# Optimization experiments

Measured on AMD Instinct MI355X. Metric: run time of the kernel, lower is better.

## Reference

```python
import jax, jax.numpy as jnp
import numpy as np

N = 100000   # nodes
E = 1600000  # edges (avg degree 16)
DN = 16      # node_attr_dim
DE = 8       # edge_attr_dim
H = 32       # node_emb_dim
L = 7        # num_gnn_layers


def setup_inputs() -> dict:
    key = jax.random.key(0)
    ks = jax.random.split(key, 8)
    s = 0.05
    return {
        "x": jax.random.normal(ks[0], (N, DN), jnp.float32),
        "edge_attr": jax.random.normal(ks[1], (E, DE), jnp.float32),
        "edge_index": jax.random.randint(ks[2], (2, E), 0, N),
        # node_init_mlp: Linear(DN -> H)
        "W_node": jax.random.normal(ks[3], (DN, H), jnp.float32) * s,
        "b_node": jnp.zeros((H,), jnp.float32),
        # per-layer message_mlp: Linear(H+DE -> H)
        "Wm": jax.random.normal(ks[4], (L, H + DE, H), jnp.float32) * s,
        "bm": jnp.zeros((L, H), jnp.float32),
        # per-layer update_mlp: Linear(H -> H) followed by ReLU
        "Wu": jax.random.normal(ks[5], (L, H, H), jnp.float32) * s,
        "bu": jnp.zeros((L, H), jnp.float32),
        # post_mlp: Linear(H -> 1)
        "W_post": jax.random.normal(ks[6], (H, 1), jnp.float32) * s,
        "b_post": jnp.zeros((1,), jnp.float32),
    }


def reference(x, edge_attr, edge_index, W_node, b_node, Wm, bm, Wu, bu, W_post, b_post):
    src = edge_index[0]  # x_j (source)
    dst = edge_index[1]  # aggregation index (target, PyG source_to_target)

    h = x @ W_node + b_node  # node_init_mlp: [N, H]

    def layer(h, params):
        Wm_l, bm_l, Wu_l, bu_l = params
        # message: concat([x_j, edge_attr]) -> Linear (extended_message_in_flag=False)
        msg_in = jnp.concatenate([h[src], edge_attr], axis=-1)  # [E, H+DE]
        msg = msg_in @ Wm_l + bm_l                              # [E, H]
        # aggregate: scatter-max onto target nodes
        aggr = jax.ops.segment_max(msg, dst, num_segments=N)    # [N, H]
        aggr = jnp.where(jnp.isneginf(aggr), 0.0, aggr)         # empty segments -> 0
        # update: ReLU(Linear(aggr)) (update_with_target_flag=False)
        upd = jax.nn.relu(aggr @ Wu_l + bu_l)
        # inter-layer bypass (residual)
        return h + upd, None

    h, _ = jax.lax.scan(layer, h, (Wm, bm, Wu, bu))
    return h @ W_post + b_post  # post_mlp: [N, 1]
```

## Files before the change

### kernel.cpp

```cpp
#include <hip/hip_runtime.h>

#define NN 100000
#define NE 1600000
#define DN 16
#define DE 8
#define H  32
#define NL 7

#define SCAN_BT   1024
#define SCAN_NB   ((NN + SCAN_BT - 1) / SCAN_BT)
#define BSUM_T    128


__global__ __launch_bounds__(256) void zero_cnt_kernel(int* __restrict__ cnt) {
    int i = blockIdx.x * blockDim.x + threadIdx.x;
    if (i < NN) cnt[i] = 0;
}

__global__ __launch_bounds__(256) void hist_kernel(const int* __restrict__ dst,
                                                   int* __restrict__ cnt) {
    int e = blockIdx.x * blockDim.x + threadIdx.x;
    if (e < NE) atomicAdd(&cnt[dst[e]], 1);
}

__global__ __launch_bounds__(SCAN_BT) void scan_partial_kernel(
        const int* __restrict__ cnt, int* __restrict__ bsum) {
    __shared__ int red[SCAN_BT];
    int t = threadIdx.x;
    int i = blockIdx.x * SCAN_BT + t;
    red[t] = (i < NN) ? cnt[i] : 0;
    __syncthreads();
    for (int off = SCAN_BT / 2; off > 0; off >>= 1) {
        if (t < off) red[t] += red[t + off];
        __syncthreads();
    }
    if (t == 0) bsum[blockIdx.x] = red[0];
}

__global__ __launch_bounds__(BSUM_T) void scan_bsum_kernel(
        const int* __restrict__ bsum, int* __restrict__ boff,
        int* __restrict__ rowstart ) {
    __shared__ int part[BSUM_T];
    int t = threadIdx.x;
    int v = (t < SCAN_NB) ? bsum[t] : 0;
    part[t] = v;
    __syncthreads();
    for (int off = 1; off < BSUM_T; off <<= 1) {
        int add = (t >= off) ? part[t - off] : 0;
        __syncthreads();
        part[t] += add;
        __syncthreads();
    }
    if (t < SCAN_NB) boff[t] = part[t] - v;
    if (t == BSUM_T - 1) rowstart[NN] = part[t];
}

__global__ __launch_bounds__(SCAN_BT) void scan_final_kernel(
        const int* __restrict__ cnt, const int* __restrict__ boff,
        int* __restrict__ rowstart, int* __restrict__ cursor) {
    __shared__ int part[SCAN_BT];
    int t = threadIdx.x;
    int i = blockIdx.x * SCAN_BT + t;
    int v = (i < NN) ? cnt[i] : 0;
    part[t] = v;
    __syncthreads();
    for (int off = 1; off < SCAN_BT; off <<= 1) {
        int add = (t >= off) ? part[t - off] : 0;
        __syncthreads();
        part[t] += add;
        __syncthreads();
    }
    if (i < NN) {
        int r = boff[blockIdx.x] + part[t] - v;
        rowstart[i] = r;
        cursor[i]   = r;
    }
}

template<int PERM>
__global__ __launch_bounds__(256) void scatter_kernel(
        const int* __restrict__ src, const int* __restrict__ dst,
        const float* __restrict__ ea,
        int* __restrict__ cursor,
        int* __restrict__ es, float* __restrict__ eas, int* __restrict__ eperm) {
    int e = blockIdx.x * blockDim.x + threadIdx.x;
    if (e >= NE) return;
    int pos = atomicAdd(&cursor[dst[e]], 1);
    es[pos] = src[e];
    if (PERM) {
        const float4* s4 = (const float4*)(ea + (long)e * DE);
        float4 a = s4[0], b = s4[1];
        float4* d4 = (float4*)(eas + (long)pos * DE);
        d4[0] = a; d4[1] = b;
    } else {
        eperm[pos] = e;
    }
}

__global__ __launch_bounds__(256) void init_kernel(
        const float* __restrict__ x,
        const float* __restrict__ W_node, const float* __restrict__ b_node,
        const float* __restrict__ Wm0, const float* __restrict__ bm0,
        float* __restrict__ h, float* __restrict__ hm)
{
    int n = blockIdx.x * blockDim.x + threadIdx.x;
    if (n >= NN) return;

    float xin[DN];
    #pragma unroll
    for (int k = 0; k < DN/4; ++k) {
        float4 v = ((const float4*)(x + (long)n*DN))[k];
        xin[4*k+0]=v.x; xin[4*k+1]=v.y; xin[4*k+2]=v.z; xin[4*k+3]=v.w;
    }
    float hv[H];
    #pragma unroll
    for (int j = 0; j < H; ++j) hv[j] = b_node[j];
    #pragma unroll
    for (int k = 0; k < DN; ++k)
        #pragma unroll
        for (int j = 0; j < H; ++j)
            hv[j] = fmaf(xin[k], W_node[k*H+j], hv[j]);

    #pragma unroll
    for (int j = 0; j < H/4; ++j)
        ((float4*)(h + (long)n*H))[j] = make_float4(hv[4*j],hv[4*j+1],hv[4*j+2],hv[4*j+3]);

    float hmv[H];
    #pragma unroll
    for (int j = 0; j < H; ++j) hmv[j] = bm0[j];
    #pragma unroll
    for (int k = 0; k < H; ++k)
        #pragma unroll
        for (int j = 0; j < H; ++j)
            hmv[j] = fmaf(hv[k], Wm0[k*H+j], hmv[j]);

    #pragma unroll
    for (int j = 0; j < H/4; ++j)
        ((float4*)(hm + (long)n*H))[j] = make_float4(hmv[4*j],hmv[4*j+1],hmv[4*j+2],hmv[4*j+3]);
}

template<int PERM>
__global__ __launch_bounds__(256) void aggr_kernel(
        const int* __restrict__ rowstart, const int* __restrict__ es,
        const float* __restrict__ eas,
        const float* __restrict__ ea,
        const int* __restrict__ eperm,
        const float* __restrict__ Wm_bot,
        const float* __restrict__ hm,
        float* __restrict__ aggr)
{
    int tid  = blockIdx.x * blockDim.x + threadIdx.x;
    int node = tid >> 4;
    int sub  = tid & 15;
    if (node >= NN) return;

    float w0[DE], w1[DE];
    #pragma unroll
    for (int k = 0; k < DE; ++k) {
        w0[k] = Wm_bot[k*H + sub*2 + 0];
        w1[k] = Wm_bot[k*H + sub*2 + 1];
    }

    float acc0 = -__builtin_inff(), acc1 = -__builtin_inff();

    int lo = rowstart[node], hi = rowstart[node+1];
    int i = lo;
    for (; i + 1 < hi; i += 2) {
        int s0 = es[i], s1 = es[i+1];
        const float4* p0;
        const float4* p1;
        if (PERM) {
            p0 = (const float4*)(eas + (long)i * DE);
            p1 = (const float4*)(eas + (long)(i+1) * DE);
        } else {
            p0 = (const float4*)(ea + (long)eperm[i] * DE);
            p1 = (const float4*)(ea + (long)eperm[i+1] * DE);
        }
        float2 hv0 = *(const float2*)(hm + (long)s0*H + sub*2);
        float2 hv1 = *(const float2*)(hm + (long)s1*H + sub*2);
        float4 a0 = p0[0], b0 = p0[1];
        float4 a1 = p1[0], b1 = p1[1];
        float m00 = hv0.x, m01 = hv0.y;
        float m10 = hv1.x, m11 = hv1.y;
        m00 = fmaf(a0.x, w0[0], m00);  m01 = fmaf(a0.x, w1[0], m01);
        m10 = fmaf(a1.x, w0[0], m10);  m11 = fmaf(a1.x, w1[0], m11);
        m00 = fmaf(a0.y, w0[1], m00);  m01 = fmaf(a0.y, w1[1], m01);
        m10 = fmaf(a1.y, w0[1], m10);  m11 = fmaf(a1.y, w1[1], m11);
        m00 = fmaf(a0.z, w0[2], m00);  m01 = fmaf(a0.z, w1[2], m01);
        m10 = fmaf(a1.z, w0[2], m10);  m11 = fmaf(a1.z, w1[2], m11);
        m00 = fmaf(a0.w, w0[3], m00);  m01 = fmaf(a0.w, w1[3], m01);
        m10 = fmaf(a1.w, w0[3], m10);  m11 = fmaf(a1.w, w1[3], m11);
        m00 = fmaf(b0.x, w0[4], m00);  m01 = fmaf(b0.x, w1[4], m01);
        m10 = fmaf(b1.x, w0[4], m10);  m11 = fmaf(b1.x, w1[4], m11);
        m00 = fmaf(b0.y, w0[5], m00);  m01 = fmaf(b0.y, w1[5], m01);
        m10 = fmaf(b1.y, w0[5], m10);  m11 = fmaf(b1.y, w1[5], m11);
        m00 = fmaf(b0.z, w0[6], m00);  m01 = fmaf(b0.z, w1[6], m01);
        m10 = fmaf(b1.z, w0[6], m10);  m11 = fmaf(b1.z, w1[6], m11);
        m00 = fmaf(b0.w, w0[7], m00);  m01 = fmaf(b0.w, w1[7], m01);
        m10 = fmaf(b1.w, w0[7], m10);  m11 = fmaf(b1.w, w1[7], m11);
        acc0 = fmaxf(acc0, fmaxf(m00, m10));
        acc1 = fmaxf(acc1, fmaxf(m01, m11));
    }
    if (i < hi) {
        int s0 = es[i];
        const float4* p0 = PERM ? (const float4*)(eas + (long)i * DE)
                                : (const float4*)(ea + (long)eperm[i] * DE);
        float2 hv0 = *(const float2*)(hm + (long)s0*H + sub*2);
        float4 a0 = p0[0], b0 = p0[1];
        float m00 = hv0.x, m01 = hv0.y;
        m00 = fmaf(a0.x, w0[0], m00);  m01 = fmaf(a0.x, w1[0], m01);
        m00 = fmaf(a0.y, w0[1], m00);  m01 = fmaf(a0.y, w1[1], m01);
        m00 = fmaf(a0.z, w0[2], m00);  m01 = fmaf(a0.z, w1[2], m01);
        m00 = fmaf(a0.w, w0[3], m00);  m01 = fmaf(a0.w, w1[3], m01);
        m00 = fmaf(b0.x, w0[4], m00);  m01 = fmaf(b0.x, w1[4], m01);
        m00 = fmaf(b0.y, w0[5], m00);  m01 = fmaf(b0.y, w1[5], m01);
        m00 = fmaf(b0.z, w0[6], m00);  m01 = fmaf(b0.z, w1[6], m01);
        m00 = fmaf(b0.w, w0[7], m00);  m01 = fmaf(b0.w, w1[7], m01);
        acc0 = fmaxf(acc0, m00);
        acc1 = fmaxf(acc1, m01);
    }
    if (lo == hi) { acc0 = 0.f; acc1 = 0.f; }
    *(float2*)(aggr + (long)node*H + sub*2) = make_float2(acc0, acc1);
}

__global__ __launch_bounds__(256) void update_kernel(
        const float* __restrict__ Wu, const float* __restrict__ bu,
        const float* __restrict__ Wm_next, const float* __restrict__ bm_next,
        const float* __restrict__ W_post, const float* __restrict__ b_post,
        float* __restrict__ h, float* __restrict__ hm,
        const float* __restrict__ aggr, float* __restrict__ out, int last)
{
    int n = blockIdx.x * blockDim.x + threadIdx.x;
    if (n >= NN) return;

    float av[H];
    #pragma unroll
    for (int j = 0; j < H/4; ++j) {
        float4 v = ((const float4*)(aggr + (long)n*H))[j];
        av[4*j+0]=v.x; av[4*j+1]=v.y; av[4*j+2]=v.z; av[4*j+3]=v.w;
    }

    float uv[H];
    #pragma unroll
    for (int j = 0; j < H; ++j) uv[j] = bu[j];
    #pragma unroll
    for (int k = 0; k < H; ++k)
        #pragma unroll
        for (int j = 0; j < H; ++j)
            uv[j] = fmaf(av[k], Wu[k*H+j], uv[j]);

    float hv[H];
    #pragma unroll
    for (int j = 0; j < H/4; ++j) {
        float4 v = ((const float4*)(h + (long)n*H))[j];
        hv[4*j+0]=v.x; hv[4*j+1]=v.y; hv[4*j+2]=v.z; hv[4*j+3]=v.w;
    }
    #pragma unroll
    for (int j = 0; j < H; ++j) hv[j] += fmaxf(uv[j], 0.f);

    #pragma unroll
    for (int j = 0; j < H/4; ++j)
        ((float4*)(h + (long)n*H))[j] = make_float4(hv[4*j],hv[4*j+1],hv[4*j+2],hv[4*j+3]);

    if (!last) {
        float hmv[H];
        #pragma unroll
        for (int j = 0; j < H; ++j) hmv[j] = bm_next[j];
        #pragma unroll
        for (int k = 0; k < H; ++k)
            #pragma unroll
            for (int j = 0; j < H; ++j)
                hmv[j] = fmaf(hv[k], Wm_next[k*H+j], hmv[j]);
        #pragma unroll
        for (int j = 0; j < H/4; ++j)
            ((float4*)(hm + (long)n*H))[j] = make_float4(hmv[4*j],hmv[4*j+1],hmv[4*j+2],hmv[4*j+3]);
    } else {
        float acc = b_post[0];
        #pragma unroll
        for (int k = 0; k < H; ++k) acc = fmaf(hv[k], W_post[k], acc);
        out[n] = acc;
    }
}

extern "C" void kernel_launch(void* const* d_in, const int* in_sizes, int n_in,
                              void* d_out, int out_size, void* d_ws, size_t ws_size,
                              hipStream_t stream)
{
    const float* x         = (const float*)d_in[0];
    const float* edge_attr = (const float*)d_in[1];
    const int*   edge_index= (const int*)  d_in[2];
    const float* W_node    = (const float*)d_in[3];
    const float* b_node    = (const float*)d_in[4];
    const float* Wm        = (const float*)d_in[5];
    const float* bm        = (const float*)d_in[6];
    const float* Wu        = (const float*)d_in[7];
    const float* bu        = (const float*)d_in[8];
    const float* W_post    = (const float*)d_in[9];
    const float* b_post    = (const float*)d_in[10];
    float* out = (float*)d_out;

    const int* src = edge_index;
    const int* dst = edge_index + NE;

    char* ws = (char*)d_ws;
    size_t off = 0;
    float* h        = (float*)(ws + off); off += (size_t)NN*H*4;
    float* hm       = (float*)(ws + off); off += (size_t)NN*H*4;
    float* aggr     = (float*)(ws + off); off += (size_t)NN*H*4;
    int*   cnt      = (int*)  (ws + off); off += (size_t)NN*4;
    int*   rowstart = (int*)  (ws + off); off += (size_t)(NN+16)*4;
    int*   cursor   = (int*)  (ws + off); off += (size_t)NN*4;
    int*   bsum     = (int*)  (ws + off); off += (size_t)256*4;
    int*   boff     = (int*)  (ws + off); off += (size_t)256*4;
    int*   es       = (int*)  (ws + off); off += (size_t)NE*4;
    size_t base = off;
    const int use_perm = (ws_size >= base + (size_t)NE*DE*4);
    float* eas   = (float*)(ws + base);
    int*   eperm = (int*)  (ws + base);

    const int nodeBlocks  = (NN + 255) / 256;
    const int edgeBlocks  = (NE + 255) / 256;
    const int aggrBlocks  = (NN*16 + 255) / 256;

    zero_cnt_kernel<<<nodeBlocks, 256, 0, stream>>>(cnt);
    hist_kernel<<<edgeBlocks, 256, 0, stream>>>(dst, cnt);
    scan_partial_kernel<<<SCAN_NB, SCAN_BT, 0, stream>>>(cnt, bsum);
    scan_bsum_kernel<<<1, BSUM_T, 0, stream>>>(bsum, boff, rowstart);
    scan_final_kernel<<<SCAN_NB, SCAN_BT, 0, stream>>>(cnt, boff, rowstart, cursor);
    if (use_perm)
        scatter_kernel<1><<<edgeBlocks, 256, 0, stream>>>(src, dst, edge_attr, cursor, es, eas, eperm);
    else
        scatter_kernel<0><<<edgeBlocks, 256, 0, stream>>>(src, dst, edge_attr, cursor, es, eas, eperm);

    init_kernel<<<nodeBlocks, 256, 0, stream>>>(x, W_node, b_node, Wm, bm, h, hm);

    for (int l = 0; l < NL; ++l) {
        const float* Wm_l   = Wm + (size_t)l*(H+DE)*H;
        const float* Wm_bot = Wm_l + (size_t)H*H;
        const float* Wu_l   = Wu + (size_t)l*H*H;
        const float* bu_l   = bu + (size_t)l*H;
        int last = (l == NL-1);
        const float* Wm_next = last ? nullptr : Wm + (size_t)(l+1)*(H+DE)*H;
        const float* bm_next = last ? nullptr : bm + (size_t)(l+1)*H;

        if (use_perm)
            aggr_kernel<1><<<aggrBlocks, 256, 0, stream>>>(rowstart, es, eas, edge_attr, eperm,
                                                           Wm_bot, hm, aggr);
        else
            aggr_kernel<0><<<aggrBlocks, 256, 0, stream>>>(rowstart, es, eas, edge_attr, eperm,
                                                           Wm_bot, hm, aggr);
        update_kernel<<<nodeBlocks, 256, 0, stream>>>(Wu_l, bu_l, Wm_next, bm_next,
                                                      W_post, b_post, h, hm, aggr, out, last);
    }
}
```

Before: 946.6 us.

## Fuse aggregation with update via subgroup shuffles; split scatter into index scatter and gather

Merges the per-layer aggregation and update kernels into one kernel. Each 16-lane group computes the node's Wu and next-layer Wm matmuls using __shfl broadcasts, which removes the aggr buffer round trip and one launch per layer. hm is double-buffered so the fused kernel can write the next layer's hm while other nodes still read the current one. When the workspace is large enough, the edge scatter is split into an atomic index-only scatter followed by a coalesced gather of src and edge_attr. This adds one extra edge pass and a permutation buffer.

```diff
diff --git a/kernel.cpp b/kernel.cpp
--- a/kernel.cpp
+++ b/kernel.cpp
@@ -77,24 +77,42 @@
     }
 }
 
-template<int PERM>
-__global__ __launch_bounds__(256) void scatter_kernel(
+__global__ __launch_bounds__(256) void scatter_idx_kernel(
+        const int* __restrict__ dst, int* __restrict__ cursor,
+        int* __restrict__ eperm) {
+    int e = blockIdx.x * blockDim.x + threadIdx.x;
+    if (e >= NE) return;
+    int pos = atomicAdd(&cursor[dst[e]], 1);
+    eperm[pos] = e;
+}
+
+__global__ __launch_bounds__(256) void gather_kernel(
+        const int* __restrict__ eperm, const int* __restrict__ src,
+        const float* __restrict__ ea,
+        int* __restrict__ es, float* __restrict__ eas) {
+    int i = blockIdx.x * blockDim.x + threadIdx.x;
+    if (i >= NE) return;
+    int e = eperm[i];
+    es[i] = src[e];
+    const float4* s4 = (const float4*)(ea + (long)e * DE);
+    float4 a = s4[0], b = s4[1];
+    float4* d4 = (float4*)(eas + (long)i * DE);
+    d4[0] = a; d4[1] = b;
+}
+
+__global__ __launch_bounds__(256) void scatter_combined_kernel(
         const int* __restrict__ src, const int* __restrict__ dst,
         const float* __restrict__ ea,
         int* __restrict__ cursor,
-        int* __restrict__ es, float* __restrict__ eas, int* __restrict__ eperm) {
+        int* __restrict__ es, float* __restrict__ eas) {
     int e = blockIdx.x * blockDim.x + threadIdx.x;
     if (e >= NE) return;
     int pos = atomicAdd(&cursor[dst[e]], 1);
     es[pos] = src[e];
-    if (PERM) {
-        const float4* s4 = (const float4*)(ea + (long)e * DE);
-        float4 a = s4[0], b = s4[1];
-        float4* d4 = (float4*)(eas + (long)pos * DE);
-        d4[0] = a; d4[1] = b;
-    } else {
-        eperm[pos] = e;
-    }
+    const float4* s4 = (const float4*)(ea + (long)e * DE);
+    float4 a = s4[0], b = s4[1];
+    float4* d4 = (float4*)(eas + (long)pos * DE);
+    d4[0] = a; d4[1] = b;
 }
 
 __global__ __launch_bounds__(256) void init_kernel(
@@ -139,15 +157,19 @@
         ((float4*)(hm + (long)n*H))[j] = make_float4(hmv[4*j],hmv[4*j+1],hmv[4*j+2],hmv[4*j+3]);
 }
 
-template<int PERM>
-__global__ __launch_bounds__(256) void aggr_kernel(
+template<int PERM, int LAST>
+__global__ __launch_bounds__(256) void aggr_update_kernel(
         const int* __restrict__ rowstart, const int* __restrict__ es,
         const float* __restrict__ eas,
         const float* __restrict__ ea,
         const int* __restrict__ eperm,
         const float* __restrict__ Wm_bot,
-        const float* __restrict__ hm,
-        float* __restrict__ aggr)
+        const float* __restrict__ hm_in,
+        const float* __restrict__ Wu, const float* __restrict__ bu,
+        const float* __restrict__ Wm_next, const float* __restrict__ bm_next,
+        const float* __restrict__ W_post, const float* __restrict__ b_post,
+        float* __restrict__ h, float* __restrict__ hm_out,
+        float* __restrict__ out)
 {
     int tid  = blockIdx.x * blockDim.x + threadIdx.x;
     int node = tid >> 4;
@@ -176,8 +198,8 @@
             p0 = (const float4*)(ea + (long)eperm[i] * DE);
             p1 = (const float4*)(ea + (long)eperm[i+1] * DE);
         }
-        float2 hv0 = *(const float2*)(hm + (long)s0*H + sub*2);
-        float2 hv1 = *(const float2*)(hm + (long)s1*H + sub*2);
+        float2 hv0 = *(const float2*)(hm_in + (long)s0*H + sub*2);
+        float2 hv1 = *(const float2*)(hm_in + (long)s1*H + sub*2);
         float4 a0 = p0[0], b0 = p0[1];
         float4 a1 = p1[0], b1 = p1[1];
         float m00 = hv0.x, m01 = hv0.y;
@@ -205,7 +227,7 @@
         int s0 = es[i];
         const float4* p0 = PERM ? (const float4*)(eas + (long)i * DE)
                                 : (const float4*)(ea + (long)eperm[i] * DE);
-        float2 hv0 = *(const float2*)(hm + (long)s0*H + sub*2);
+        float2 hv0 = *(const float2*)(hm_in + (long)s0*H + sub*2);
         float4 a0 = p0[0], b0 = p0[1];
         float m00 = hv0.x, m01 = hv0.y;
         m00 = fmaf(a0.x, w0[0], m00);  m01 = fmaf(a0.x, w1[0], m01);
@@ -220,65 +242,39 @@
         acc1 = fmaxf(acc1, m01);
     }
     if (lo == hi) { acc0 = 0.f; acc1 = 0.f; }
-    *(float2*)(aggr + (long)node*H + sub*2) = make_float2(acc0, acc1);
-}
-
-__global__ __launch_bounds__(256) void update_kernel(
-        const float* __restrict__ Wu, const float* __restrict__ bu,
-        const float* __restrict__ Wm_next, const float* __restrict__ bm_next,
-        const float* __restrict__ W_post, const float* __restrict__ b_post,
-        float* __restrict__ h, float* __restrict__ hm,
-        const float* __restrict__ aggr, float* __restrict__ out, int last)
-{
-    int n = blockIdx.x * blockDim.x + threadIdx.x;
-    if (n >= NN) return;
-
-    float av[H];
-    #pragma unroll
-    for (int j = 0; j < H/4; ++j) {
-        float4 v = ((const float4*)(aggr + (long)n*H))[j];
-        av[4*j+0]=v.x; av[4*j+1]=v.y; av[4*j+2]=v.z; av[4*j+3]=v.w;
-    }
-
-    float uv[H];
-    #pragma unroll
-    for (int j = 0; j < H; ++j) uv[j] = bu[j];
-    #pragma unroll
-    for (int k = 0; k < H; ++k)
+
+    float uv0 = bu[2*sub+0], uv1 = bu[2*sub+1];
+    #pragma unroll
+    for (int k = 0; k < 16; ++k) {
+        float a0 = __shfl(acc0, k, 16);
+        float a1 = __shfl(acc1, k, 16);
+        float2 wA = *(const float2*)(Wu + (2*k+0)*H + 2*sub);
+        float2 wB = *(const float2*)(Wu + (2*k+1)*H + 2*sub);
+        uv0 = fmaf(a0, wA.x, uv0); uv1 = fmaf(a0, wA.y, uv1);
+        uv0 = fmaf(a1, wB.x, uv0); uv1 = fmaf(a1, wB.y, uv1);
+    }
+    float2 hrow = *(const float2*)(h + (long)node*H + 2*sub);
+    float hv0 = hrow.x + fmaxf(uv0, 0.f);
+    float hv1 = hrow.y + fmaxf(uv1, 0.f);
+    *(float2*)(h + (long)node*H + 2*sub) = make_float2(hv0, hv1);
+
+    if (!LAST) {
+        float m0 = bm_next[2*sub+0], m1 = bm_next[2*sub+1];
         #pragma unroll
-        for (int j = 0; j < H; ++j)
-            uv[j] = fmaf(av[k], Wu[k*H+j], uv[j]);
-
-    float hv[H];
-    #pragma unroll
-    for (int j = 0; j < H/4; ++j) {
-        float4 v = ((const float4*)(h + (long)n*H))[j];
-        hv[4*j+0]=v.x; hv[4*j+1]=v.y; hv[4*j+2]=v.z; hv[4*j+3]=v.w;
-    }
-    #pragma unroll
-    for (int j = 0; j < H; ++j) hv[j] += fmaxf(uv[j], 0.f);
-
-    #pragma unroll
-    for (int j = 0; j < H/4; ++j)
-        ((float4*)(h + (long)n*H))[j] = make_float4(hv[4*j],hv[4*j+1],hv[4*j+2],hv[4*j+3]);
-
-    if (!last) {
-        float hmv[H];
+        for (int k = 0; k < 16; ++k) {
+            float a0 = __shfl(hv0, k, 16);
+            float a1 = __shfl(hv1, k, 16);
+            float2 wA = *(const float2*)(Wm_next + (2*k+0)*H + 2*sub);
+            float2 wB = *(const float2*)(Wm_next + (2*k+1)*H + 2*sub);
+            m0 = fmaf(a0, wA.x, m0); m1 = fmaf(a0, wA.y, m1);
+            m0 = fmaf(a1, wB.x, m0); m1 = fmaf(a1, wB.y, m1);
+        }
+        *(float2*)(hm_out + (long)node*H + 2*sub) = make_float2(m0, m1);
+    } else {
+        float p = hv0 * W_post[2*sub+0] + hv1 * W_post[2*sub+1];
         #pragma unroll
-        for (int j = 0; j < H; ++j) hmv[j] = bm_next[j];
-        #pragma unroll
-        for (int k = 0; k < H; ++k)
-            #pragma unroll
-            for (int j = 0; j < H; ++j)
-                hmv[j] = fmaf(hv[k], Wm_next[k*H+j], hmv[j]);
-        #pragma unroll
-        for (int j = 0; j < H/4; ++j)
-            ((float4*)(hm + (long)n*H))[j] = make_float4(hmv[4*j],hmv[4*j+1],hmv[4*j+2],hmv[4*j+3]);
-    } else {
-        float acc = b_post[0];
-        #pragma unroll
-        for (int k = 0; k < H; ++k) acc = fmaf(hv[k], W_post[k], acc);
-        out[n] = acc;
+        for (int o = 8; o >= 1; o >>= 1) p += __shfl_xor(p, o, 16);
+        if (sub == 0) out[node] = p + b_post[0];
     }
 }
 
@@ -305,8 +301,8 @@
     char* ws = (char*)d_ws;
     size_t off = 0;
     float* h        = (float*)(ws + off); off += (size_t)NN*H*4;
-    float* hm       = (float*)(ws + off); off += (size_t)NN*H*4;
-    float* aggr     = (float*)(ws + off); off += (size_t)NN*H*4;
+    float* hm0      = (float*)(ws + off); off += (size_t)NN*H*4;
+    float* hm1      = (float*)(ws + off); off += (size_t)NN*H*4;
     int*   cnt      = (int*)  (ws + off); off += (size_t)NN*4;
     int*   rowstart = (int*)  (ws + off); off += (size_t)(NN+16)*4;
     int*   cursor   = (int*)  (ws + off); off += (size_t)NN*4;
@@ -314,9 +310,17 @@
     int*   boff     = (int*)  (ws + off); off += (size_t)256*4;
     int*   es       = (int*)  (ws + off); off += (size_t)NE*4;
     size_t base = off;
-    const int use_perm = (ws_size >= base + (size_t)NE*DE*4);
+
+    int mode;
     float* eas   = (float*)(ws + base);
-    int*   eperm = (int*)  (ws + base);
+    int*   eperm = nullptr;
+    if (ws_size >= base + (size_t)NE*DE*4 + (size_t)NE*4) {
+        mode = 2; eperm = (int*)(ws + base + (size_t)NE*DE*4);
+    } else if (ws_size >= base + (size_t)NE*DE*4) {
+        mode = 1;
+    } else {
+        mode = 0; eperm = (int*)(ws + base);
+    }
 
     const int nodeBlocks  = (NN + 255) / 256;
     const int edgeBlocks  = (NE + 255) / 256;
@@ -327,12 +331,18 @@
     scan_partial_kernel<<<SCAN_NB, SCAN_BT, 0, stream>>>(cnt, bsum);
     scan_bsum_kernel<<<1, BSUM_T, 0, stream>>>(bsum, boff, rowstart);
     scan_final_kernel<<<SCAN_NB, SCAN_BT, 0, stream>>>(cnt, boff, rowstart, cursor);
-    if (use_perm)
-        scatter_kernel<1><<<edgeBlocks, 256, 0, stream>>>(src, dst, edge_attr, cursor, es, eas, eperm);
-    else
-        scatter_kernel<0><<<edgeBlocks, 256, 0, stream>>>(src, dst, edge_attr, cursor, es, eas, eperm);
-
-    init_kernel<<<nodeBlocks, 256, 0, stream>>>(x, W_node, b_node, Wm, bm, h, hm);
+    if (mode == 2) {
+        scatter_idx_kernel<<<edgeBlocks, 256, 0, stream>>>(dst, cursor, eperm);
+        gather_kernel<<<edgeBlocks, 256, 0, stream>>>(eperm, src, edge_attr, es, eas);
+    } else if (mode == 1) {
+        scatter_combined_kernel<<<edgeBlocks, 256, 0, stream>>>(src, dst, edge_attr,
+                                                                cursor, es, eas);
+    } else {
+        scatter_idx_kernel<<<edgeBlocks, 256, 0, stream>>>(dst, cursor, eperm);
+        gather_kernel<<<edgeBlocks, 256, 0, stream>>>(eperm, src, edge_attr, es, eas);
+    }
+
+    init_kernel<<<nodeBlocks, 256, 0, stream>>>(x, W_node, b_node, Wm, bm, h, hm0);
 
     for (int l = 0; l < NL; ++l) {
         const float* Wm_l   = Wm + (size_t)l*(H+DE)*H;
@@ -342,14 +352,27 @@
         int last = (l == NL-1);
         const float* Wm_next = last ? nullptr : Wm + (size_t)(l+1)*(H+DE)*H;
         const float* bm_next = last ? nullptr : bm + (size_t)(l+1)*H;
-
-        if (use_perm)
-            aggr_kernel<1><<<aggrBlocks, 256, 0, stream>>>(rowstart, es, eas, edge_attr, eperm,
-                                                           Wm_bot, hm, aggr);
-        else
-            aggr_kernel<0><<<aggrBlocks, 256, 0, stream>>>(rowstart, es, eas, edge_attr, eperm,
-                                                           Wm_bot, hm, aggr);
-        update_kernel<<<nodeBlocks, 256, 0, stream>>>(Wu_l, bu_l, Wm_next, bm_next,
-                                                      W_post, b_post, h, hm, aggr, out, last);
-    }
-}
+        float* hm_in  = (l & 1) ? hm1 : hm0;
+        float* hm_out = (l & 1) ? hm0 : hm1;
+
+        if (mode >= 1) {
+            if (last)
+                aggr_update_kernel<1,1><<<aggrBlocks, 256, 0, stream>>>(
+                    rowstart, es, eas, edge_attr, eperm, Wm_bot, hm_in,
+                    Wu_l, bu_l, Wm_next, bm_next, W_post, b_post, h, hm_out, out);
+            else
+                aggr_update_kernel<1,0><<<aggrBlocks, 256, 0, stream>>>(
+                    rowstart, es, eas, edge_attr, eperm, Wm_bot, hm_in,
+                    Wu_l, bu_l, Wm_next, bm_next, W_post, b_post, h, hm_out, out);
+        } else {
+            if (last)
+                aggr_update_kernel<0,1><<<aggrBlocks, 256, 0, stream>>>(
+                    rowstart, es, eas, edge_attr, eperm, Wm_bot, hm_in,
+                    Wu_l, bu_l, Wm_next, bm_next, W_post, b_post, h, hm_out, out);
+            else
+                aggr_update_kernel<0,0><<<aggrBlocks, 256, 0, stream>>>(
+                    rowstart, es, eas, edge_attr, eperm, Wm_bot, hm_in,
+                    Wu_l, bu_l, Wm_next, bm_next, W_post, b_post, h, hm_out, out);
+        }
+    }
+}
```

New measurement: 1.122 ms. 1.19x slower.
